# Performance work log

Hardware: AMD Instinct MI355X
Metric: run time of the kernel (lower is better)

Reference implementation:

```python
import jax, jax.numpy as jnp
import numpy as np

ISIZE = 1024
OSIZE = 1024
EPS = 1e-5  # torch nn.LayerNorm default


def setup_inputs() -> dict:
    key = jax.random.key(0)
    k0, k1, k2 = jax.random.split(key, 3)
    B, S = 32, 256
    x = jax.random.normal(k0, (B, S, ISIZE), dtype=jnp.float32)
    # Linear(isize + osize, 4*osize): W stored as (in, out) for x @ W
    scale = 1.0 / np.sqrt(ISIZE + OSIZE)
    W = jax.random.uniform(k1, (ISIZE + OSIZE, 4 * OSIZE), dtype=jnp.float32,
                           minval=-scale, maxval=scale)
    b = jax.random.uniform(k2, (4 * OSIZE,), dtype=jnp.float32,
                           minval=-scale, maxval=scale)
    gamma = jnp.ones((4, OSIZE), dtype=jnp.float32)   # LayerNorm((4, osize)) weight
    beta = jnp.zeros((4, OSIZE), dtype=jnp.float32)   # LayerNorm((4, osize)) bias
    init_hx = jnp.zeros((1, OSIZE), dtype=jnp.float32)
    init_cx = jnp.zeros((1, OSIZE), dtype=jnp.float32)
    return {"x": x, "W": W, "b": b, "gamma": gamma, "beta": beta,
            "init_hx": init_hx, "init_cx": init_cx}


def _layernorm_2d(z, gamma, beta):
    # Normalize jointly over the last two dims (4, osize), per torch LayerNorm((4, osize))
    mean = jnp.mean(z, axis=(-2, -1), keepdims=True)
    var = jnp.var(z, axis=(-2, -1), keepdims=True)
    return (z - mean) * jax.lax.rsqrt(var + EPS) * gamma + beta


def reference(x, W, b, gamma, beta, init_hx, init_cx):
    B, S, _ = x.shape
    osize = init_hx.shape[-1]
    hx = jnp.broadcast_to(init_hx, (B, osize))  # prepare_initState: expand to batch
    cx = jnp.broadcast_to(init_cx, (B, osize))

    def step(carry, xt):
        h, c = carry
        comb = jnp.concatenate([xt, h], axis=-1) @ W + b       # [B, 4*osize]
        comb = _layernorm_2d(comb.reshape(B, 4, osize), gamma, beta)
        ig, fg, hidden, og = comb[:, 0], comb[:, 1], comb[:, 2], comb[:, 3]
        c = jax.nn.sigmoid(fg) * c + jax.nn.sigmoid(ig) * jnp.tanh(hidden)
        h = jax.nn.sigmoid(og) * c                              # RNMT+ cell: out = og * cell
        return (h, c), h

    xs = jnp.swapaxes(x, 0, 1)                                  # [S, B, isize]
    _, outs = jax.lax.scan(step, (hx, cx), xs)
    return jnp.swapaxes(outs, 0, 1)                             # [B, S, osize]
```

## Files before the change

kernel.cpp:

```cpp
#include <hip/hip_runtime.h>
#include <hip/hip_bf16.h>

#define NB 32
#define NS 256
#define NI 1024
#define NO 1024
#define NK 2048
#define NC 4096
#define LN_EPS 1e-5f

typedef __attribute__((ext_vector_type(4))) float f32x4;
typedef __attribute__((ext_vector_type(4))) unsigned int u32x4;

__device__ __forceinline__ f32x4 mfma_bf16_16x16x32(u32x4 a, u32x4 b, f32x4 c) {
  asm volatile("v_mfma_f32_16x16x32_bf16 %0, %1, %2, %0" : "+v"(c) : "v"(a), "v"(b));
  return c;
}

__device__ __forceinline__ float sigf(float x) { return 1.0f / (1.0f + __expf(-x)); }
__device__ __forceinline__ float tanhfast(float x) {
  return 1.0f - 2.0f / (__expf(2.0f * x) + 1.0f);
}


__global__ void pack_x(const float* __restrict__ x, __hip_bfloat16* __restrict__ xfrag) {
  const int t = blockIdx.x, kt = blockIdx.y;
  const int tid = threadIdx.x;
  const int plane = tid >> 6, l = tid & 63, q = (l >> 4), ln = l & 15;
  const int m = plane * 16 + ln;
  const float* src = x + ((size_t)m * NS + t) * NI + kt * 32 + q * 8;
  float4 v0 = *(const float4*)src;
  float4 v1 = *(const float4*)(src + 4);
  __align__(16) __hip_bfloat16 tmp[8];
  tmp[0] = __float2bfloat16(v0.x); tmp[1] = __float2bfloat16(v0.y);
  tmp[2] = __float2bfloat16(v0.z); tmp[3] = __float2bfloat16(v0.w);
  tmp[4] = __float2bfloat16(v1.x); tmp[5] = __float2bfloat16(v1.y);
  tmp[6] = __float2bfloat16(v1.z); tmp[7] = __float2bfloat16(v1.w);
  *(u32x4*)(xfrag + (((size_t)t * 32 + kt) * 2 + plane) * 512 + l * 8) = *(const u32x4*)tmp;
}

__global__ void pack_wf(const float* __restrict__ W, __hip_bfloat16* __restrict__ WF) {
  const int blk = blockIdx.x;
  const int b = blk >> 6, kt = blk & 63;
  const int l = threadIdx.x, q = l >> 4, c = l & 15;
  const int n  = ((c >> 2) << 10) + b * 4 + (c & 3);
  const int k0 = kt * 32 + q * 8;
  __align__(16) __hip_bfloat16 tmp[8];
#pragma unroll
  for (int j = 0; j < 8; ++j)
    tmp[j] = __float2bfloat16(W[(size_t)(k0 + j) * NC + n]);
  *(u32x4*)(WF + ((size_t)(b * 64 + kt) * 64 + l) * 8) = *(const u32x4*)tmp;
}

__device__ __forceinline__ size_t hfrag_idx(int m, int j) {
  const int kt = j >> 5, q = (j >> 3) & 3, jj = j & 7;
  const int plane = m >> 4, l = q * 16 + (m & 15);
  return (((size_t)kt * 2 + plane) * 64 + l) * 8 + jj;
}

__global__ void init_state(const float* __restrict__ hx0, const float* __restrict__ cx0,
                           __hip_bfloat16* __restrict__ hfrag, float* __restrict__ cst,
                           float* __restrict__ hf) {
  const int i = blockIdx.x * 256 + threadIdx.x;
  const int m = i >> 10, j = i & (NO - 1);
  const float hv = hx0[j];
  hfrag[hfrag_idx(m, j)] = __float2bfloat16(hv);
  hf[i]  = hv;
  cst[i] = cx0[j];
}

__global__ __launch_bounds__(512)
void precompute_xw(const __hip_bfloat16* __restrict__ xfrag,
                   const __hip_bfloat16* __restrict__ WF,
                   const float* __restrict__ bias,
                   float* __restrict__ xw) {
  const int tq = blockIdx.x, nb = blockIdx.y;
  const int tid = threadIdx.x;
  const int w = tid >> 6, l = tid & 63, q = l >> 4, c = l & 15;
  const int tp = w >> 2, ng = w & 3;
  const int t0  = tq * 4 + tp * 2;
  const int bg0 = nb * 8 + ng * 2;

  float bias_g[2];
#pragma unroll
  for (int g = 0; g < 2; ++g)
    bias_g[g] = bias[((c >> 2) << 10) + (bg0 + g) * 4 + (c & 3)];

  f32x4 acc[2][2][2] = {};
  asm volatile("s_nop 1" ::);
  for (int kt = 0; kt < 32; ++kt) {
    u32x4 a[2][2], bb[2];
#pragma unroll
    for (int tt = 0; tt < 2; ++tt)
#pragma unroll
      for (int p = 0; p < 2; ++p)
        a[tt][p] = *(const u32x4*)(xfrag +
            (((size_t)(t0 + tt) * 32 + kt) * 2 + p) * 512 + l * 8);
#pragma unroll
    for (int g = 0; g < 2; ++g)
      bb[g] = *(const u32x4*)(WF + (((size_t)(bg0 + g) * 64 + kt) * 64 + l) * 8);
#pragma unroll
    for (int tt = 0; tt < 2; ++tt)
#pragma unroll
      for (int p = 0; p < 2; ++p)
#pragma unroll
        for (int g = 0; g < 2; ++g)
          acc[tt][p][g] = mfma_bf16_16x16x32(a[tt][p], bb[g], acc[tt][p][g]);
  }
  asm volatile("s_nop 7\n\ts_nop 7" ::);
#pragma unroll
  for (int tt = 0; tt < 2; ++tt)
#pragma unroll
    for (int p = 0; p < 2; ++p)
#pragma unroll
      for (int g = 0; g < 2; ++g) {
        const int n = ((c >> 2) << 10) + (bg0 + g) * 4 + (c & 3);
#pragma unroll
        for (int r = 0; r < 4; ++r) {
          const int row = p * 16 + q * 4 + r;
          xw[((size_t)(t0 + tt) * 32 + row) * NC + n] = acc[tt][p][g][r] + bias_g[g];
        }
      }
}

__global__ __launch_bounds__(512)
void step_gemm_h(const __hip_bfloat16* __restrict__ hfrag,
                 const __hip_bfloat16* __restrict__ WF,
                 const float* __restrict__ xw,
                 float* __restrict__ comb, int t) {
  __shared__ __align__(16) float xch[8 * 256];
  const int b = blockIdx.x, tid = threadIdx.x;
  const int w = tid >> 6, l = tid & 63;
  const int p = w & 1, k0 = (w >> 1) * 8;

  const __hip_bfloat16* ap = hfrag + ((size_t)k0 * 2 + p) * 512 + l * 8;
  const __hip_bfloat16* bp = WF + (((size_t)b * 64 + 32 + k0) * 64 + l) * 8;

  f32x4 acc = {0.f, 0.f, 0.f, 0.f};
  asm volatile("s_nop 1" ::);
#pragma unroll
  for (int i = 0; i < 8; ++i) {
    u32x4 a  = *(const u32x4*)(ap + (size_t)i * 1024);
    u32x4 bb = *(const u32x4*)(bp + (size_t)i * 512);
    acc = mfma_bf16_16x16x32(a, bb, acc);
  }
  asm volatile("s_nop 7\n\ts_nop 7" ::);

  *(f32x4*)(xch + w * 256 + l * 4) = acc;
  __syncthreads();

  const int row = tid >> 4, c = tid & 15;
  const int pp = row >> 4, rr = row & 15;
  const int idx = ((rr >> 2) * 16 + c) * 4 + (rr & 3);
  const int n = ((c >> 2) << 10) + b * 4 + (c & 3);
  float v = xw[((size_t)t * 32 + row) * NC + n];
#pragma unroll
  for (int i = 0; i < 4; ++i) v += xch[(i * 2 + pp) * 256 + idx];
  comb[(size_t)row * NC + n] = v;
}

__global__ __launch_bounds__(512)
void step_gemm_mfma(const __hip_bfloat16* __restrict__ xfrag,
                    const __hip_bfloat16* __restrict__ hfrag,
                    const __hip_bfloat16* __restrict__ WF,
                    const float* __restrict__ bias,
                    float* __restrict__ comb, int t) {
  __shared__ __align__(16) float xch[8 * 2 * 256];
  const int b = blockIdx.x, tid = threadIdx.x;
  const int wv = tid >> 6, l = tid & 63;

  const __hip_bfloat16* ap = (wv < 4)
      ? xfrag + ((size_t)t * 32 + wv * 8) * 1024 + l * 8
      : hfrag + ((size_t)(wv - 4) * 8) * 1024 + l * 8;
  const __hip_bfloat16* bp = WF + ((size_t)(b * 64 + wv * 8) * 64 + l) * 8;

  f32x4 acc0 = {0.f, 0.f, 0.f, 0.f}, acc1 = {0.f, 0.f, 0.f, 0.f};
  asm volatile("s_nop 1" ::);
#pragma unroll
  for (int i = 0; i < 8; ++i) {
    u32x4 a0 = *(const u32x4*)(ap + (size_t)i * 1024);
    u32x4 a1 = *(const u32x4*)(ap + (size_t)i * 1024 + 512);
    u32x4 bb = *(const u32x4*)(bp + (size_t)i * 512);
    acc0 = mfma_bf16_16x16x32(a0, bb, acc0);
    acc1 = mfma_bf16_16x16x32(a1, bb, acc1);
  }
  asm volatile("s_nop 7\n\ts_nop 7" ::);

  *(f32x4*)(xch + (wv * 2 + 0) * 256 + l * 4) = acc0;
  *(f32x4*)(xch + (wv * 2 + 1) * 256 + l * 4) = acc1;
  __syncthreads();

  const int row = tid >> 4, c = tid & 15;
  const int p = row >> 4, rr = row & 15;
  const int idx = ((rr >> 2) * 16 + c) * 4 + (rr & 3);
  const int n = ((c >> 2) << 10) + b * 4 + (c & 3);
  float v = bias[n];
#pragma unroll
  for (int w = 0; w < 8; ++w) v += xch[(w * 2 + p) * 256 + idx];
  comb[(size_t)row * NC + n] = v;
}

__global__ __launch_bounds__(1024)
void step_update_row(const float* __restrict__ comb,
                     const float* __restrict__ gamma,
                     const float* __restrict__ beta,
                     float* __restrict__ cst,
                     float* __restrict__ out,
                     __hip_bfloat16* __restrict__ hfrag,
                     int t) {
  __shared__ __align__(16) float combL[NC];
  __shared__ float red[16][2];
  __shared__ float stat[2];
  const int m = blockIdx.x, tid = threadIdx.x;

  f32x4 cv = *(const f32x4*)(comb + (size_t)m * NC + tid * 4);
  *(f32x4*)(combL + tid * 4) = cv;
  float s  = cv[0] + cv[1] + cv[2] + cv[3];
  float ss = cv[0] * cv[0] + cv[1] * cv[1] + cv[2] * cv[2] + cv[3] * cv[3];
#pragma unroll
  for (int off = 1; off < 64; off <<= 1) {
    s  += __shfl_xor(s, off);
    ss += __shfl_xor(ss, off);
  }
  const int wid = tid >> 6;
  if ((tid & 63) == 0) { red[wid][0] = s; red[wid][1] = ss; }
  __syncthreads();
  if (tid == 0) {
    float s2 = 0.f, ss2 = 0.f;
#pragma unroll
    for (int i = 0; i < 16; ++i) { s2 += red[i][0]; ss2 += red[i][1]; }
    const float mean = s2 * (1.f / NC);
    const float var  = ss2 * (1.f / NC) - mean * mean;
    stat[0] = mean;
    stat[1] = rsqrtf(var + LN_EPS);
  }
  __syncthreads();
  const float mean = stat[0], rs = stat[1];
  const int j = tid;
  const float iv = (combL[j]          - mean) * rs * gamma[j]          + beta[j];
  const float fv = (combL[NO + j]     - mean) * rs * gamma[NO + j]     + beta[NO + j];
  const float gv = (combL[2 * NO + j] - mean) * rs * gamma[2 * NO + j] + beta[2 * NO + j];
  const float ov = (combL[3 * NO + j] - mean) * rs * gamma[3 * NO + j] + beta[3 * NO + j];
  const float cold = cst[(size_t)m * NO + j];
  const float cc = sigf(fv) * cold + sigf(iv) * tanhfast(gv);
  const float hh = sigf(ov) * cc;
  cst[(size_t)m * NO + j] = cc;
  out[((size_t)m * NS + t) * NO + j] = hh;
  hfrag[hfrag_idx(m, j)] = __float2bfloat16(hh);
}


__launch_bounds__(256)
__global__ void step_gemm_f32(const float* __restrict__ x, const float* __restrict__ hf,
                              const float* __restrict__ W, const float* __restrict__ bias,
                              float* __restrict__ comb, int t) {
  const int blk = blockIdx.x;
  const int tid = threadIdx.x;
  const int n   = blk * 16 + (tid & 15);
  const int mlo = tid >> 4;
  float a0 = 0.f, a1 = 0.f;
  for (int k = 0; k < NI; ++k) {
    const float wv = W[(size_t)k * NC + n];
    a0 += x[((size_t)mlo * NS + t) * NI + k] * wv;
    a1 += x[((size_t)(mlo + 16) * NS + t) * NI + k] * wv;
  }
  for (int k = 0; k < NO; ++k) {
    const float wv = W[(size_t)(NI + k) * NC + n];
    a0 += hf[mlo * NO + k] * wv;
    a1 += hf[(mlo + 16) * NO + k] * wv;
  }
  comb[(size_t)mlo * NC + n] = a0 + bias[n];
  comb[(size_t)(mlo + 16) * NC + n] = a1 + bias[n];
}

__global__ __launch_bounds__(1024)
void step_update_row_f32(const float* __restrict__ comb,
                         const float* __restrict__ gamma,
                         const float* __restrict__ beta,
                         float* __restrict__ cst,
                         float* __restrict__ out,
                         float* __restrict__ hf,
                         int t) {
  __shared__ __align__(16) float combL[NC];
  __shared__ float red[16][2];
  __shared__ float stat[2];
  const int m = blockIdx.x, tid = threadIdx.x;
  f32x4 cv = *(const f32x4*)(comb + (size_t)m * NC + tid * 4);
  *(f32x4*)(combL + tid * 4) = cv;
  float s  = cv[0] + cv[1] + cv[2] + cv[3];
  float ss = cv[0] * cv[0] + cv[1] * cv[1] + cv[2] * cv[2] + cv[3] * cv[3];
#pragma unroll
  for (int off = 1; off < 64; off <<= 1) {
    s  += __shfl_xor(s, off);
    ss += __shfl_xor(ss, off);
  }
  const int wid = tid >> 6;
  if ((tid & 63) == 0) { red[wid][0] = s; red[wid][1] = ss; }
  __syncthreads();
  if (tid == 0) {
    float s2 = 0.f, ss2 = 0.f;
    for (int i = 0; i < 16; ++i) { s2 += red[i][0]; ss2 += red[i][1]; }
    const float mean = s2 * (1.f / NC);
    const float var  = ss2 * (1.f / NC) - mean * mean;
    stat[0] = mean;
    stat[1] = rsqrtf(var + LN_EPS);
  }
  __syncthreads();
  const float mean = stat[0], rs = stat[1];
  const int j = tid;
  const float iv = (combL[j]          - mean) * rs * gamma[j]          + beta[j];
  const float fv = (combL[NO + j]     - mean) * rs * gamma[NO + j]     + beta[NO + j];
  const float gv = (combL[2 * NO + j] - mean) * rs * gamma[2 * NO + j] + beta[2 * NO + j];
  const float ov = (combL[3 * NO + j] - mean) * rs * gamma[3 * NO + j] + beta[3 * NO + j];
  const float cold = cst[(size_t)m * NO + j];
  const float cc = sigf(fv) * cold + sigf(iv) * tanhfast(gv);
  const float hh = sigf(ov) * cc;
  cst[(size_t)m * NO + j] = cc;
  out[((size_t)m * NS + t) * NO + j] = hh;
  hf[(size_t)m * NO + j] = hh;
}


extern "C" void kernel_launch(void* const* d_in, const int* in_sizes, int n_in,
                              void* d_out, int out_size, void* d_ws, size_t ws_size,
                              hipStream_t stream) {
  (void)in_sizes; (void)n_in; (void)out_size;
  const float* x     = (const float*)d_in[0];
  const float* W     = (const float*)d_in[1];
  const float* bias  = (const float*)d_in[2];
  const float* gamma = (const float*)d_in[3];
  const float* beta  = (const float*)d_in[4];
  const float* hx0   = (const float*)d_in[5];
  const float* cx0   = (const float*)d_in[6];
  float* outp = (float*)d_out;

  char* ws = (char*)d_ws;
  size_t off = 0;
  auto alloc = [&](size_t bytes) -> char* {
    off = (off + 255) & ~(size_t)255;
    char* p = ws + off;
    off += bytes;
    return p;
  };
  float* comb           = (float*)alloc((size_t)NB * NC * 4);
  float* cst            = (float*)alloc((size_t)NB * NO * 4);
  float* hf             = (float*)alloc((size_t)NB * NO * 4);
  __hip_bfloat16* hfrag = (__hip_bfloat16*)alloc((size_t)NB * NO * 2);
  __hip_bfloat16* xfrag = (__hip_bfloat16*)alloc((size_t)NB * NS * NI * 2);
  __hip_bfloat16* WF    = (__hip_bfloat16*)alloc((size_t)NK * NC * 2);
  const size_t off_mid = off;
  float* xw             = (float*)alloc((size_t)NS * NB * NC * 4);
  const size_t off_full = off;
  const int tier = (ws_size >= off_full) ? 2 : (ws_size >= off_mid) ? 1 : 0;

  hipLaunchKernelGGL(init_state, dim3((NB * NO) / 256), dim3(256), 0, stream,
                     hx0, cx0, hfrag, cst, hf);
  if (tier == 2) {
    hipLaunchKernelGGL(pack_x, dim3(NS, 32), dim3(128), 0, stream, x, xfrag);
    hipLaunchKernelGGL(pack_wf, dim3(256 * 64), dim3(64), 0, stream, W, WF);
    hipLaunchKernelGGL(precompute_xw, dim3(64, 32), dim3(512), 0, stream,
                       xfrag, WF, bias, xw);
    for (int t = 0; t < NS; ++t) {
      hipLaunchKernelGGL(step_gemm_h, dim3(256), dim3(512), 0, stream,
                         hfrag, WF, xw, comb, t);
      hipLaunchKernelGGL(step_update_row, dim3(NB), dim3(1024), 0, stream,
                         comb, gamma, beta, cst, outp, hfrag, t);
    }
  } else if (tier == 1) {
    hipLaunchKernelGGL(pack_x, dim3(NS, 32), dim3(128), 0, stream, x, xfrag);
    hipLaunchKernelGGL(pack_wf, dim3(256 * 64), dim3(64), 0, stream, W, WF);
    for (int t = 0; t < NS; ++t) {
      hipLaunchKernelGGL(step_gemm_mfma, dim3(256), dim3(512), 0, stream,
                         xfrag, hfrag, WF, bias, comb, t);
      hipLaunchKernelGGL(step_update_row, dim3(NB), dim3(1024), 0, stream,
                         comb, gamma, beta, cst, outp, hfrag, t);
    }
  } else {
    for (int t = 0; t < NS; ++t) {
      hipLaunchKernelGGL(step_gemm_f32, dim3(256), dim3(256), 0, stream,
                         x, hf, W, bias, comb, t);
      hipLaunchKernelGGL(step_update_row_f32, dim3(NB), dim3(1024), 0, stream,
                         comb, gamma, beta, cst, outp, hf, t);
    }
  }
}
```

Baseline: 2.506 ms.

## Fuse recurrent GEMM with LayerNorm/gate update into one kernel per step

Each timestep previously ran two kernels: the h-GEMM and a row-wise LayerNorm plus gate update. These are merged into one fused kernel per step. Every block recomputes the full h for its 16 rows from the previous step's fp16 pre-activations and partial LN statistics, then does its slice of the GEMM and writes new partial sums. This halves the launches and drops the separate update pass, at the cost of redundant gate math in every block, fp16 storage of pre-activations and cell state (less precision), and a tail kernel for the last step.

```diff
diff --git a/kernel.cpp b/kernel.cpp
--- a/kernel.cpp
+++ b/kernel.cpp
@@ -1,5 +1,6 @@
 #include <hip/hip_runtime.h>
 #include <hip/hip_bf16.h>
+#include <hip/hip_fp16.h>
 
 #define NB 32
 #define NS 256
@@ -11,15 +12,24 @@
 
 typedef __attribute__((ext_vector_type(4))) float f32x4;
 typedef __attribute__((ext_vector_type(4))) unsigned int u32x4;
+typedef __attribute__((ext_vector_type(8))) _Float16 f16x8;
 
 __device__ __forceinline__ f32x4 mfma_bf16_16x16x32(u32x4 a, u32x4 b, f32x4 c) {
   asm volatile("v_mfma_f32_16x16x32_bf16 %0, %1, %2, %0" : "+v"(c) : "v"(a), "v"(b));
   return c;
 }
 
-__device__ __forceinline__ float sigf(float x) { return 1.0f / (1.0f + __expf(-x)); }
+__device__ __forceinline__ float sigf(float x) {
+  return __builtin_amdgcn_rcpf(1.0f + __expf(-x));
+}
 __device__ __forceinline__ float tanhfast(float x) {
-  return 1.0f - 2.0f / (__expf(2.0f * x) + 1.0f);
+  return 1.0f - 2.0f * __builtin_amdgcn_rcpf(__expf(2.0f * x) + 1.0f);
+}
+
+__device__ __forceinline__ unsigned short bf16u(float f) {
+  union { float f; unsigned int u; } v; v.f = f;
+  unsigned int r = (v.u + 0x7fff + ((v.u >> 16) & 1)) >> 16;
+  return (unsigned short)r;
 }
 
 
@@ -60,13 +70,14 @@
 
 __global__ void init_state(const float* __restrict__ hx0, const float* __restrict__ cx0,
                            __hip_bfloat16* __restrict__ hfrag, float* __restrict__ cst,
-                           float* __restrict__ hf) {
+                           float* __restrict__ hf, _Float16* __restrict__ cH0) {
   const int i = blockIdx.x * 256 + threadIdx.x;
   const int m = i >> 10, j = i & (NO - 1);
   const float hv = hx0[j];
   hfrag[hfrag_idx(m, j)] = __float2bfloat16(hv);
   hf[i]  = hv;
   cst[i] = cx0[j];
+  cH0[i] = (_Float16)cx0[j];
 }
 
 __global__ __launch_bounds__(512)
@@ -124,40 +135,187 @@
 }
 
 __global__ __launch_bounds__(512)
-void step_gemm_h(const __hip_bfloat16* __restrict__ hfrag,
-                 const __hip_bfloat16* __restrict__ WF,
-                 const float* __restrict__ xw,
-                 float* __restrict__ comb, int t) {
-  __shared__ __align__(16) float xch[8 * 256];
-  const int b = blockIdx.x, tid = threadIdx.x;
-  const int w = tid >> 6, l = tid & 63;
-  const int p = w & 1, k0 = (w >> 1) * 8;
-
-  const __hip_bfloat16* ap = hfrag + ((size_t)k0 * 2 + p) * 512 + l * 8;
-  const __hip_bfloat16* bp = WF + (((size_t)b * 64 + 32 + k0) * 64 + l) * 8;
-
-  f32x4 acc = {0.f, 0.f, 0.f, 0.f};
-  asm volatile("s_nop 1" ::);
-#pragma unroll
-  for (int i = 0; i < 8; ++i) {
-    u32x4 a  = *(const u32x4*)(ap + (size_t)i * 1024);
-    u32x4 bb = *(const u32x4*)(bp + (size_t)i * 512);
-    acc = mfma_bf16_16x16x32(a, bb, acc);
-  }
-  asm volatile("s_nop 7\n\ts_nop 7" ::);
-
-  *(f32x4*)(xch + w * 256 + l * 4) = acc;
-  __syncthreads();
-
-  const int row = tid >> 4, c = tid & 15;
-  const int pp = row >> 4, rr = row & 15;
-  const int idx = ((rr >> 2) * 16 + c) * 4 + (rr & 3);
-  const int n = ((c >> 2) << 10) + b * 4 + (c & 3);
-  float v = xw[((size_t)t * 32 + row) * NC + n];
-#pragma unroll
-  for (int i = 0; i < 4; ++i) v += xch[(i * 2 + pp) * 256 + idx];
-  comb[(size_t)row * NC + n] = v;
-}
+void fused_step(const _Float16* __restrict__ comb_prev,
+                _Float16* __restrict__ comb_new,
+                const _Float16* __restrict__ c_prev,
+                _Float16* __restrict__ c_new,
+                const float* __restrict__ part_prev,
+                float* __restrict__ part_new,
+                const __hip_bfloat16* __restrict__ WF,
+                const float* __restrict__ xw,
+                const float* __restrict__ gamma,
+                const float* __restrict__ beta,
+                const float* __restrict__ hx0,
+                float* __restrict__ out,
+                int t) {
+  __shared__ __align__(16) unsigned short hfragL[32 * 65 * 8];
+  __shared__ __align__(16) float xchL[8][2][256];
+  __shared__ float statL[16][2];
+
+  const int mp = blockIdx.x & 1, nb = blockIdx.x >> 1;
+  const int tid = threadIdx.x;
+
+  if (t > 0) {
+    {
+      const int row = tid >> 5, rr = tid & 31;
+      const float* pp = part_prev + ((size_t)(mp * 16 + row) * 128 + rr * 4) * 2;
+      f32x4 v1 = *(const f32x4*)pp;
+      f32x4 v2 = *(const f32x4*)(pp + 4);
+      float s  = v1[0] + v1[2] + v2[0] + v2[2];
+      float ss = v1[1] + v1[3] + v2[1] + v2[3];
+      s += __shfl_xor(s, 1);  ss += __shfl_xor(ss, 1);
+      s += __shfl_xor(s, 2);  ss += __shfl_xor(ss, 2);
+      s += __shfl_xor(s, 4);  ss += __shfl_xor(ss, 4);
+      s += __shfl_xor(s, 8);  ss += __shfl_xor(ss, 8);
+      s += __shfl_xor(s, 16); ss += __shfl_xor(ss, 16);
+      if (rr == 0) {
+        const float mean = s * (1.f / NC);
+        const float var  = ss * (1.f / NC) - mean * mean;
+        statL[row][0] = mean;
+        statL[row][1] = rsqrtf(var + LN_EPS);
+      }
+    }
+    __syncthreads();
+
+    const int m16 = tid >> 5, r = tid & 31;
+    const int m = mp * 16 + m16;
+    const float mean = statL[m16][0], rstd = statL[m16][1];
+#pragma unroll
+    for (int i = 0; i < 4; ++i) {
+      const int j0 = i * 256 + r * 8;
+      float av[4][8];
+#pragma unroll
+      for (int g = 0; g < 4; ++g) {
+        f16x8 cb = *(const f16x8*)(comb_prev + (size_t)m * NC + g * 1024 + j0);
+        f32x4 ga = *(const f32x4*)(gamma + g * 1024 + j0);
+        f32x4 gb = *(const f32x4*)(gamma + g * 1024 + j0 + 4);
+        f32x4 ba = *(const f32x4*)(beta  + g * 1024 + j0);
+        f32x4 bb = *(const f32x4*)(beta  + g * 1024 + j0 + 4);
+#pragma unroll
+        for (int jj = 0; jj < 4; ++jj) {
+          av[g][jj]     = ((float)cb[jj]     - mean) * rstd * ga[jj] + ba[jj];
+          av[g][jj + 4] = ((float)cb[jj + 4] - mean) * rstd * gb[jj] + bb[jj];
+        }
+      }
+      f16x8 c8 = *(const f16x8*)(c_prev + (size_t)m * NO + j0);
+      __align__(16) unsigned short hb[8];
+      _Float16 cn8[8];
+      float hf_[8];
+#pragma unroll
+      for (int jj = 0; jj < 8; ++jj) {
+        const float cn = sigf(av[1][jj]) * (float)c8[jj] + sigf(av[0][jj]) * tanhfast(av[2][jj]);
+        const float hh = sigf(av[3][jj]) * cn;
+        cn8[jj] = (_Float16)cn;
+        hf_[jj] = hh;
+        hb[jj]  = bf16u(hh);
+      }
+      const int slot = (i * 8 + (r >> 2)) * 65 + (r & 3) * 16 + m16;
+      *(u32x4*)(hfragL + (size_t)slot * 8) = *(const u32x4*)hb;
+      if ((i * 32 + r) == nb) {
+        float* op = out + ((size_t)m * NS + (t - 1)) * NO + j0;
+#pragma unroll
+        for (int jj = 0; jj < 8; ++jj) op[jj] = hf_[jj];
+        *(u32x4*)(c_new + (size_t)m * NO + j0) = *(const u32x4*)cn8;
+      }
+    }
+  } else {
+    const int m16 = tid >> 5, r = tid & 31;
+#pragma unroll
+    for (int i = 0; i < 4; ++i) {
+      const int j0 = i * 256 + r * 8;
+      f32x4 v0 = *(const f32x4*)(hx0 + j0);
+      f32x4 v1 = *(const f32x4*)(hx0 + j0 + 4);
+      __align__(16) unsigned short hb[8];
+#pragma unroll
+      for (int jj = 0; jj < 4; ++jj) { hb[jj] = bf16u(v0[jj]); hb[jj + 4] = bf16u(v1[jj]); }
+      const int slot = (i * 8 + (r >> 2)) * 65 + (r & 3) * 16 + m16;
+      *(u32x4*)(hfragL + (size_t)slot * 8) = *(const u32x4*)hb;
+    }
+  }
+  __syncthreads();
+
+  {
+    const int w = tid >> 6, l = tid & 63;
+    f32x4 acc0 = {0.f, 0.f, 0.f, 0.f}, acc1 = {0.f, 0.f, 0.f, 0.f};
+    asm volatile("s_nop 1" ::);
+#pragma unroll
+    for (int i = 0; i < 4; ++i) {
+      const int kt = w * 4 + i;
+      u32x4 a  = *(const u32x4*)(hfragL + ((size_t)kt * 65 + l) * 8);
+      u32x4 b0 = *(const u32x4*)(WF + (((size_t)(2 * nb + 0) * 64 + 32 + kt) * 64 + l) * 8);
+      u32x4 b1 = *(const u32x4*)(WF + (((size_t)(2 * nb + 1) * 64 + 32 + kt) * 64 + l) * 8);
+      acc0 = mfma_bf16_16x16x32(a, b0, acc0);
+      acc1 = mfma_bf16_16x16x32(a, b1, acc1);
+    }
+    asm volatile("s_nop 7\n\ts_nop 7" ::);
+    *(f32x4*)(&xchL[w][0][l * 4]) = acc0;
+    *(f32x4*)(&xchL[w][1][l * 4]) = acc1;
+  }
+  __syncthreads();
+
+  {
+    const int row = tid >> 5, nc = tid & 31;
+    const int g = nc >> 4, c = nc & 15;
+    const int idx = ((row >> 2) * 16 + c) * 4 + (row & 3);
+    const int n = ((c >> 2) << 10) + (2 * nb + g) * 4 + (c & 3);
+    const int m = mp * 16 + row;
+    float v = xw[((size_t)t * 32 + m) * NC + n];
+#pragma unroll
+    for (int w = 0; w < 8; ++w) v += xchL[w][g][idx];
+    comb_new[(size_t)m * NC + n] = (_Float16)v;
+    float s = v, ss = v * v;
+    s += __shfl_xor(s, 1);  ss += __shfl_xor(ss, 1);
+    s += __shfl_xor(s, 2);  ss += __shfl_xor(ss, 2);
+    s += __shfl_xor(s, 4);  ss += __shfl_xor(ss, 4);
+    s += __shfl_xor(s, 8);  ss += __shfl_xor(ss, 8);
+    s += __shfl_xor(s, 16); ss += __shfl_xor(ss, 16);
+    if (nc == 0) {
+      float* pp = part_new + ((size_t)m * 128 + nb) * 2;
+      pp[0] = s; pp[1] = ss;
+    }
+  }
+}
+
+__global__ __launch_bounds__(1024)
+void final_update(const _Float16* __restrict__ comb,
+                  const _Float16* __restrict__ cprev,
+                  const float* __restrict__ part,
+                  const float* __restrict__ gamma,
+                  const float* __restrict__ beta,
+                  float* __restrict__ out) {
+  __shared__ float wsum[2][2];
+  __shared__ float stat[2];
+  const int m = blockIdx.x, tid = threadIdx.x;
+  if (tid < 128) {
+    const float* pp = part + ((size_t)m * 128 + tid) * 2;
+    float s = pp[0], ss = pp[1];
+    s += __shfl_xor(s, 1);  ss += __shfl_xor(ss, 1);
+    s += __shfl_xor(s, 2);  ss += __shfl_xor(ss, 2);
+    s += __shfl_xor(s, 4);  ss += __shfl_xor(ss, 4);
+    s += __shfl_xor(s, 8);  ss += __shfl_xor(ss, 8);
+    s += __shfl_xor(s, 16); ss += __shfl_xor(ss, 16);
+    s += __shfl_xor(s, 32); ss += __shfl_xor(ss, 32);
+    if ((tid & 63) == 0) { wsum[tid >> 6][0] = s; wsum[tid >> 6][1] = ss; }
+  }
+  __syncthreads();
+  if (tid == 0) {
+    const float s = wsum[0][0] + wsum[1][0], ss = wsum[0][1] + wsum[1][1];
+    const float mean = s * (1.f / NC);
+    const float var  = ss * (1.f / NC) - mean * mean;
+    stat[0] = mean;
+    stat[1] = rsqrtf(var + LN_EPS);
+  }
+  __syncthreads();
+  const float mean = stat[0], rstd = stat[1];
+  const int j = tid;
+  const float iv = ((float)comb[(size_t)m * NC + j]          - mean) * rstd * gamma[j]          + beta[j];
+  const float fv = ((float)comb[(size_t)m * NC + NO + j]     - mean) * rstd * gamma[NO + j]     + beta[NO + j];
+  const float gv = ((float)comb[(size_t)m * NC + 2 * NO + j] - mean) * rstd * gamma[2 * NO + j] + beta[2 * NO + j];
+  const float ov = ((float)comb[(size_t)m * NC + 3 * NO + j] - mean) * rstd * gamma[3 * NO + j] + beta[3 * NO + j];
+  const float cn = sigf(fv) * (float)cprev[(size_t)m * NO + j] + sigf(iv) * tanhfast(gv);
+  out[((size_t)m * NS + (NS - 1)) * NO + j] = sigf(ov) * cn;
+}
+
 
 __global__ __launch_bounds__(512)
 void step_gemm_mfma(const __hip_bfloat16* __restrict__ xfrag,
@@ -168,12 +326,10 @@
   __shared__ __align__(16) float xch[8 * 2 * 256];
   const int b = blockIdx.x, tid = threadIdx.x;
   const int wv = tid >> 6, l = tid & 63;
-
   const __hip_bfloat16* ap = (wv < 4)
       ? xfrag + ((size_t)t * 32 + wv * 8) * 1024 + l * 8
       : hfrag + ((size_t)(wv - 4) * 8) * 1024 + l * 8;
   const __hip_bfloat16* bp = WF + ((size_t)(b * 64 + wv * 8) * 64 + l) * 8;
-
   f32x4 acc0 = {0.f, 0.f, 0.f, 0.f}, acc1 = {0.f, 0.f, 0.f, 0.f};
   asm volatile("s_nop 1" ::);
 #pragma unroll
@@ -185,11 +341,9 @@
     acc1 = mfma_bf16_16x16x32(a1, bb, acc1);
   }
   asm volatile("s_nop 7\n\ts_nop 7" ::);
-
   *(f32x4*)(xch + (wv * 2 + 0) * 256 + l * 4) = acc0;
   *(f32x4*)(xch + (wv * 2 + 1) * 256 + l * 4) = acc1;
   __syncthreads();
-
   const int row = tid >> 4, c = tid & 15;
   const int p = row >> 4, rr = row & 15;
   const int idx = ((rr >> 2) * 16 + c) * 4 + (rr & 3);
@@ -212,7 +366,6 @@
   __shared__ float red[16][2];
   __shared__ float stat[2];
   const int m = blockIdx.x, tid = threadIdx.x;
-
   f32x4 cv = *(const f32x4*)(comb + (size_t)m * NC + tid * 4);
   *(f32x4*)(combL + tid * 4) = cv;
   float s  = cv[0] + cv[1] + cv[2] + cv[3];
@@ -346,6 +499,15 @@
   float* cst            = (float*)alloc((size_t)NB * NO * 4);
   float* hf             = (float*)alloc((size_t)NB * NO * 4);
   __hip_bfloat16* hfrag = (__hip_bfloat16*)alloc((size_t)NB * NO * 2);
+  _Float16* combH[2];
+  combH[0] = (_Float16*)alloc((size_t)NB * NC * 2);
+  combH[1] = (_Float16*)alloc((size_t)NB * NC * 2);
+  _Float16* cH[2];
+  cH[0] = (_Float16*)alloc((size_t)NB * NO * 2);
+  cH[1] = (_Float16*)alloc((size_t)NB * NO * 2);
+  float* part[2];
+  part[0] = (float*)alloc((size_t)NB * 128 * 2 * 4);
+  part[1] = (float*)alloc((size_t)NB * 128 * 2 * 4);
   __hip_bfloat16* xfrag = (__hip_bfloat16*)alloc((size_t)NB * NS * NI * 2);
   __hip_bfloat16* WF    = (__hip_bfloat16*)alloc((size_t)NK * NC * 2);
   const size_t off_mid = off;
@@ -354,18 +516,24 @@
   const int tier = (ws_size >= off_full) ? 2 : (ws_size >= off_mid) ? 1 : 0;
 
   hipLaunchKernelGGL(init_state, dim3((NB * NO) / 256), dim3(256), 0, stream,
-                     hx0, cx0, hfrag, cst, hf);
+                     hx0, cx0, hfrag, cst, hf, cH[0]);
   if (tier == 2) {
     hipLaunchKernelGGL(pack_x, dim3(NS, 32), dim3(128), 0, stream, x, xfrag);
     hipLaunchKernelGGL(pack_wf, dim3(256 * 64), dim3(64), 0, stream, W, WF);
     hipLaunchKernelGGL(precompute_xw, dim3(64, 32), dim3(512), 0, stream,
                        xfrag, WF, bias, xw);
     for (int t = 0; t < NS; ++t) {
-      hipLaunchKernelGGL(step_gemm_h, dim3(256), dim3(512), 0, stream,
-                         hfrag, WF, xw, comb, t);
-      hipLaunchKernelGGL(step_update_row, dim3(NB), dim3(1024), 0, stream,
-                         comb, gamma, beta, cst, outp, hfrag, t);
-    }
+      const int pr = (t + 1) & 1, pw = t & 1;
+      hipLaunchKernelGGL(fused_step, dim3(256), dim3(512), 0, stream,
+                         (const _Float16*)combH[pr], combH[pw],
+                         (const _Float16*)cH[pr], cH[pw],
+                         (const float*)part[pr], part[pw],
+                         (const __hip_bfloat16*)WF, (const float*)xw,
+                         gamma, beta, hx0, outp, t);
+    }
+    hipLaunchKernelGGL(final_update, dim3(NB), dim3(1024), 0, stream,
+                       (const _Float16*)combH[1], (const _Float16*)cH[1],
+                       (const float*)part[1], gamma, beta, outp);
   } else if (tier == 1) {
     hipLaunchKernelGGL(pack_x, dim3(NS, 32), dim3(128), 0, stream, x, xfrag);
     hipLaunchKernelGGL(pack_wf, dim3(256 * 64), dim3(64), 0, stream, W, WF);
```

After: 3.565 ms. 42.3% more time.
